# Kernel optimization log

Hardware: AMD Instinct MI355X
Metric: run time of the kernel (lower is better)

## Reference

```python
import math
import jax, jax.numpy as jnp
import numpy as np

BH, S, DK = 64, 1024, 64   # batch*heads, seq_len, head dim
FG, FL = 32, 32            # global / local enrichment feature dims
H, B = 16, 4               # mask layout [heads, batch, seq]


def setup_inputs() -> dict:
    key = jax.random.key(0)
    k1, k2, k3, k4, k5, k6 = jax.random.split(key, 6)
    return {
        "query": jax.random.normal(k1, (BH, S, DK), dtype=jnp.float32),
        "key": jax.random.normal(k2, (BH, S, DK), dtype=jnp.float32),
        "value": jax.random.normal(k3, (BH, S, DK), dtype=jnp.float32),
        "local_f": jax.random.normal(k4, (BH, S, FL), dtype=jnp.float32),
        "global_f": jax.random.normal(k5, (BH, S, FG), dtype=jnp.float32),
        "mask": jax.random.randint(k6, (H, B, S), 0, 2, dtype=jnp.int32),
    }


def reference(query, key, value, local_f, global_f, mask):
    dk = query.shape[-1]
    # enrich q/k with global then local features (matches torch concat order)
    pq = jnp.concatenate([query, global_f, local_f], axis=2)   # [BH, S, dk+fg+fl]
    pk = jnp.concatenate([key, global_f, local_f], axis=2)
    scores = jnp.einsum("bqd,bkd->bqk", pq, pk) / math.sqrt(dk)  # [BH, S, S]
    # mask [H, B, S] -> [H*B, S] -> broadcast over query positions
    m = mask.reshape(-1, mask.shape[-1])[:, None, :]            # [H*B, 1, S]
    scores = jnp.where(m == 1, jnp.float32(-1e9), scores)
    attn = jax.nn.softmax(scores, axis=-1)
    return jnp.einsum("bqk,bkd->bqd", attn, value)              # [BH, S, dk]
```

## Files before the change

kernel.cpp:

```cpp
#include <hip/hip_runtime.h>
#include <hip/hip_bf16.h>


#define BHn 64
#define Sn  1024
#define NT  16
#define KSTR 144
#define VSTR 72
#define KTILE (64*KSTR*2)
#define VTILE (64*VSTR*2)
#define OSTR 68
#define SMEMB (128*OSTR*4 + 512)

typedef __attribute__((ext_vector_type(8)))  __bf16 bf16x8;
typedef __attribute__((ext_vector_type(16))) float  f32x16;
typedef __attribute__((ext_vector_type(4)))  unsigned int u32x4;

__device__ __forceinline__ unsigned f2bf1(float a){
    union { float f; unsigned u; } c; c.f = a;
    return (c.u + 0x7fffu + ((c.u >> 16) & 1u)) >> 16;
}
__device__ __forceinline__ unsigned f2bf2(float a, float b){
    return f2bf1(a) | (f2bf1(b) << 16);
}
__device__ __forceinline__ unsigned pkbf(float a, float b){
    return __builtin_amdgcn_perm(__builtin_bit_cast(unsigned, b),
                                 __builtin_bit_cast(unsigned, a), 0x07060302u);
}
__device__ __forceinline__ void gld_lds16(const void* g, void* l){
    __builtin_amdgcn_global_load_lds(
        (const __attribute__((address_space(1))) unsigned int*)g,
        (__attribute__((address_space(3))) unsigned int*)l, 16, 0, 0);
}

__global__ __launch_bounds__(256)
void attn_prep(const float* __restrict__ K, const float* __restrict__ V,
               const float* __restrict__ LF, const float* __restrict__ GF,
               const int* __restrict__ M,
               unsigned short* __restrict__ Kp, unsigned short* __restrict__ Vp)
{
    const int tid = threadIdx.x;
    const int bh = blockIdx.x >> 4, ti = blockIdx.x & 15, kb = ti*64;
    unsigned short* ktg = Kp + (size_t)(bh*NT + ti) * (64*KSTR);
    unsigned int*   vtg = (unsigned int*)(Vp + (size_t)(bh*NT + ti) * (64*VSTR));

    #pragma unroll
    for (int i=0;i<2;i++){
        int idx = tid + 256*i, row = idx>>3, c = idx&7;
        const float* s = K + ((size_t)bh*Sn + kb + row)*64 + c*8;
        float4 f0 = *(const float4*)s, f1 = *(const float4*)(s+4);
        u32x4 w; w[0]=f2bf2(f0.x,f0.y); w[1]=f2bf2(f0.z,f0.w);
        w[2]=f2bf2(f1.x,f1.y); w[3]=f2bf2(f1.z,f1.w);
        *(u32x4*)(ktg + row*KSTR + c*8) = w;
    }
    {
        int row = tid>>2, c = tid&3;
        const float* s = GF + ((size_t)bh*Sn + kb + row)*32 + c*8;
        float4 f0 = *(const float4*)s, f1 = *(const float4*)(s+4);
        u32x4 w; w[0]=f2bf2(f0.x,f0.y); w[1]=f2bf2(f0.z,f0.w);
        w[2]=f2bf2(f1.x,f1.y); w[3]=f2bf2(f1.z,f1.w);
        *(u32x4*)(ktg + row*KSTR + 64 + c*8) = w;
    }
    {
        int row = tid>>2, c = tid&3;
        const float* s = LF + ((size_t)bh*Sn + kb + row)*32 + c*8;
        float4 f0 = *(const float4*)s, f1 = *(const float4*)(s+4);
        u32x4 w; w[0]=f2bf2(f0.x,f0.y); w[1]=f2bf2(f0.z,f0.w);
        w[2]=f2bf2(f1.x,f1.y); w[3]=f2bf2(f1.z,f1.w);
        *(u32x4*)(ktg + row*KSTR + 96 + c*8) = w;
    }
    if (tid < 64){
        int mv = M[(size_t)bh*Sn + kb + tid];
        u32x4 w; w[0] = (mv == 1) ? 0x0000ceacu : 0u;
        w[1]=0u; w[2]=0u; w[3]=0u;
        *(u32x4*)(ktg + tid*KSTR + 128) = w;
        u32x4 z; z[0]=0u; z[1]=0u; z[2]=0u; z[3]=0u;
        *(u32x4*)(ktg + tid*KSTR + 136) = z;
    }
    {
        int d = tid & 63, g = tid >> 6;
        const float* vb = V + ((size_t)bh*Sn + kb + 16*g)*64 + d;
        const int pm[16] = {0,1,2,3, 8,9,10,11, 4,5,6,7, 12,13,14,15};
        unsigned w[8];
        #pragma unroll
        for (int m=0;m<8;m++)
            w[m] = f2bf2(vb[(size_t)pm[2*m]*64], vb[(size_t)pm[2*m+1]*64]);
        u32x4 a, b;
        a[0]=w[0]; a[1]=w[1]; a[2]=w[2]; a[3]=w[3];
        b[0]=w[4]; b[1]=w[5]; b[2]=w[6]; b[3]=w[7];
        *(u32x4*)(vtg + d*36 + g*8)     = a;
        *(u32x4*)(vtg + d*36 + g*8 + 4) = b;
    }
}

__global__ __launch_bounds__(512, 4)
void attn_main(const float* __restrict__ Q, const unsigned short* __restrict__ Kp,
               const unsigned short* __restrict__ Vp,
               const float* __restrict__ GF, const float* __restrict__ LF,
               float* __restrict__ O)
{
    __shared__ __align__(16) unsigned char smem[SMEMB];
    unsigned short* kt_s = (unsigned short*)smem;
    unsigned short* vt_s = (unsigned short*)(smem + KTILE);

    const int tid  = threadIdx.x;
    const int wave = tid >> 6, lane = tid & 63;
    const int l31  = lane & 31, h = lane >> 5;
    const int qh   = wave >> 1;
    const int kp   = wave & 1;
    const int bh = blockIdx.x & 63;
    const int qb = blockIdx.x >> 6;
    const float SCL = 0.18033688011112042f;

    const int qrow = qb*128 + qh*32 + l31;
    u32x4 qf[9];
    #pragma unroll
    for (int dc = 0; dc < 8; dc++){
        const int cb = dc*16 + 8*h;
        const float* src;
        if (cb < 64)      src = Q  + ((size_t)bh*Sn + qrow)*64 + cb;
        else if (cb < 96) src = GF + ((size_t)bh*Sn + qrow)*32 + (cb - 64);
        else              src = LF + ((size_t)bh*Sn + qrow)*32 + (cb - 96);
        float4 f0 = *(const float4*)src;
        float4 f1 = *(const float4*)(src + 4);
        qf[dc][0] = f2bf2(f0.x*SCL, f0.y*SCL);
        qf[dc][1] = f2bf2(f0.z*SCL, f0.w*SCL);
        qf[dc][2] = f2bf2(f1.x*SCL, f1.y*SCL);
        qf[dc][3] = f2bf2(f1.z*SCL, f1.w*SCL);
    }
    qf[8][0] = h ? 0u : 0x00003f80u;
    qf[8][1] = 0u; qf[8][2] = 0u; qf[8][3] = 0u;

    f32x16 oacc[2];
    #pragma unroll
    for (int dt=0; dt<2; dt++)
        #pragma unroll
        for (int r=0; r<16; r++) oacc[dt][r] = 0.f;
    float lrun = 0.f;

    for (int t = 0; t < NT; t++){
        __syncthreads();
        const unsigned char* gK = (const unsigned char*)Kp + (size_t)(bh*NT + t)*KTILE;
        const unsigned char* gV = (const unsigned char*)Vp + (size_t)(bh*NT + t)*VTILE;
        #pragma unroll
        for (int i=0;i<4;i++){
            int c = wave + 8*i;
            if (c < 18)      gld_lds16(gK + (size_t)c*1024 + lane*16, smem + c*1024);
            else if (c < 27) gld_lds16(gV + (size_t)(c-18)*1024 + lane*16,
                                       smem + KTILE + (size_t)(c-18)*1024);
        }
        __syncthreads();

        f32x16 acc;
        #pragma unroll
        for (int r=0;r<16;r++) acc[r] = 0.f;
        #pragma unroll
        for (int dc=0; dc<9; dc++){
            u32x4 ar = *(const u32x4*)(kt_s + (kp*32 + l31)*KSTR + dc*16 + 8*h);
            acc = __builtin_amdgcn_mfma_f32_32x32x16_bf16(
                    __builtin_bit_cast(bf16x8, ar),
                    __builtin_bit_cast(bf16x8, qf[dc]), acc, 0, 0, 0);
        }

        float rs = 0.f;
        #pragma unroll
        for (int r=0;r<16;r++){
            float p = __builtin_amdgcn_exp2f(acc[r]);
            acc[r] = p; rs += p;
        }
        lrun += rs;

        unsigned pk[8];
        #pragma unroll
        for (int i=0;i<8;i++) pk[i] = pkbf(acc[2*i], acc[2*i+1]);
        u32x4 b0, b1;
        b0[0]=pk[0]; b0[1]=pk[1]; b0[2]=pk[2]; b0[3]=pk[3];
        b1[0]=pk[4]; b1[1]=pk[5]; b1[2]=pk[6]; b1[3]=pk[7];

        #pragma unroll
        for (int dt=0;dt<2;dt++){
            u32x4 va0 = *(const u32x4*)(vt_s + (dt*32 + l31)*VSTR + kp*32 + 8*h);
            u32x4 va1 = *(const u32x4*)(vt_s + (dt*32 + l31)*VSTR + kp*32 + 16 + 8*h);
            oacc[dt] = __builtin_amdgcn_mfma_f32_32x32x16_bf16(
                    __builtin_bit_cast(bf16x8, va0),
                    __builtin_bit_cast(bf16x8, b0), oacc[dt], 0, 0, 0);
            oacc[dt] = __builtin_amdgcn_mfma_f32_32x32x16_bf16(
                    __builtin_bit_cast(bf16x8, va1),
                    __builtin_bit_cast(bf16x8, b1), oacc[dt], 0, 0, 0);
        }
    }

    __syncthreads();
    float lw = lrun + __shfl_xor(lrun, 32, 64);
    float* s1 = (float*)smem;
    float* s2 = (float*)(smem + 128*OSTR*4);
    if (kp == 1){
        #pragma unroll
        for (int dt=0;dt<2;dt++)
            #pragma unroll
            for (int rg=0;rg<4;rg++){
                float4 w;
                w.x = oacc[dt][rg*4+0]; w.y = oacc[dt][rg*4+1];
                w.z = oacc[dt][rg*4+2]; w.w = oacc[dt][rg*4+3];
                *(float4*)(s1 + (qh*32 + l31)*OSTR + dt*32 + rg*8 + 4*h) = w;
            }
        if (h == 0) s2[qh*32 + l31] = lw;
    }
    __syncthreads();
    if (kp == 0){
        float inv = 1.0f / (lw + s2[qh*32 + l31]);
        #pragma unroll
        for (int dt=0;dt<2;dt++)
            #pragma unroll
            for (int rg=0;rg<4;rg++){
                float* p = s1 + (qh*32 + l31)*OSTR + dt*32 + rg*8 + 4*h;
                float4 w = *(float4*)p;
                w.x = (w.x + oacc[dt][rg*4+0])*inv;
                w.y = (w.y + oacc[dt][rg*4+1])*inv;
                w.z = (w.z + oacc[dt][rg*4+2])*inv;
                w.w = (w.w + oacc[dt][rg*4+3])*inv;
                *(float4*)p = w;
            }
    }
    __syncthreads();
    #pragma unroll
    for (int i=0;i<4;i++){
        int idx = tid + 512*i, r = idx>>4, c = idx&15;
        *(float4*)(O + ((size_t)bh*Sn + qb*128 + r)*64 + c*4) =
            *(const float4*)(s1 + r*OSTR + c*4);
    }
}

extern "C" void kernel_launch(void* const* d_in, const int* in_sizes, int n_in,
                              void* d_out, int out_size, void* d_ws, size_t ws_size,
                              hipStream_t stream) {
    const float* Q  = (const float*)d_in[0];
    const float* K  = (const float*)d_in[1];
    const float* V  = (const float*)d_in[2];
    const float* LF = (const float*)d_in[3];
    const float* GF = (const float*)d_in[4];
    const int*   M  = (const int*)d_in[5];
    float* O = (float*)d_out;

    unsigned short* Kp = (unsigned short*)d_ws;
    unsigned short* Vp = Kp + (size_t)BHn*NT*64*KSTR;

    attn_prep<<<dim3(BHn*NT), dim3(256), 0, stream>>>(K, V, LF, GF, M, Kp, Vp);
    attn_main<<<dim3(BHn*(Sn/128)), dim3(512), 0, stream>>>(Q, Kp, Vp, GF, LF, O);
}
```

Measured before the change: 148.7 us.

## Double-buffer K/V tile loads into LDS and widen K row stride

Splits shared memory into two K/V buffers. The global-to-LDS load for tile t+1 is issued before computing on tile t, with a vmcnt wait at the end of each iteration, so load latency overlaps with the MFMA work. Also pads the packed K row stride from 144 to 152 elements, likely to reduce LDS bank conflicts, and zero-fills the extra padding in the prep kernel. LDS use per block grows to about 57 KB, which limits how many blocks fit on a CU.

```diff
diff --git a/kernel.cpp b/kernel.cpp
--- a/kernel.cpp
+++ b/kernel.cpp
@@ -5,12 +5,13 @@
 #define BHn 64
 #define Sn  1024
 #define NT  16
-#define KSTR 144
+#define KSTR 152
 #define VSTR 72
 #define KTILE (64*KSTR*2)
 #define VTILE (64*VSTR*2)
+#define BUFSZ (KTILE+VTILE)
 #define OSTR 68
-#define SMEMB (128*OSTR*4 + 512)
+#define WAIT_VM0 0x0F70
 
 typedef __attribute__((ext_vector_type(8)))  __bf16 bf16x8;
 typedef __attribute__((ext_vector_type(16))) float  f32x16;
@@ -76,6 +77,7 @@
         *(u32x4*)(ktg + tid*KSTR + 128) = w;
         u32x4 z; z[0]=0u; z[1]=0u; z[2]=0u; z[3]=0u;
         *(u32x4*)(ktg + tid*KSTR + 136) = z;
+        *(u32x4*)(ktg + tid*KSTR + 144) = z;
     }
     {
         int d = tid & 63, g = tid >> 6;
@@ -99,10 +101,7 @@
                const float* __restrict__ GF, const float* __restrict__ LF,
                float* __restrict__ O)
 {
-    __shared__ __align__(16) unsigned char smem[SMEMB];
-    unsigned short* kt_s = (unsigned short*)smem;
-    unsigned short* vt_s = (unsigned short*)(smem + KTILE);
-
+    __shared__ __align__(16) unsigned char smem[2*BUFSZ];
     const int tid  = threadIdx.x;
     const int wave = tid >> 6, lane = tid & 63;
     const int l31  = lane & 31, h = lane >> 5;
@@ -138,18 +137,37 @@
         for (int r=0; r<16; r++) oacc[dt][r] = 0.f;
     float lrun = 0.f;
 
-    for (int t = 0; t < NT; t++){
-        __syncthreads();
-        const unsigned char* gK = (const unsigned char*)Kp + (size_t)(bh*NT + t)*KTILE;
-        const unsigned char* gV = (const unsigned char*)Vp + (size_t)(bh*NT + t)*VTILE;
+    const unsigned char* gKb = (const unsigned char*)Kp + (size_t)bh*NT*KTILE;
+    const unsigned char* gVb = (const unsigned char*)Vp + (size_t)bh*NT*VTILE;
+
+    {
         #pragma unroll
         for (int i=0;i<4;i++){
             int c = wave + 8*i;
-            if (c < 18)      gld_lds16(gK + (size_t)c*1024 + lane*16, smem + c*1024);
-            else if (c < 27) gld_lds16(gV + (size_t)(c-18)*1024 + lane*16,
-                                       smem + KTILE + (size_t)(c-18)*1024);
-        }
+            if (c < 19)      gld_lds16(gKb + (size_t)c*1024 + lane*16, smem + c*1024);
+            else if (c < 28) gld_lds16(gVb + (size_t)(c-19)*1024 + lane*16,
+                                       smem + KTILE + (size_t)(c-19)*1024);
+        }
+    }
+    __builtin_amdgcn_s_waitcnt(WAIT_VM0);
+
+    for (int t = 0; t < NT; t++){
+        unsigned char* cur = smem + (size_t)(t&1)*BUFSZ;
+        unsigned char* nxt = smem + (size_t)((t+1)&1)*BUFSZ;
         __syncthreads();
+        if (t+1 < NT){
+            const unsigned char* gK = gKb + (size_t)(t+1)*KTILE;
+            const unsigned char* gV = gVb + (size_t)(t+1)*VTILE;
+            #pragma unroll
+            for (int i=0;i<4;i++){
+                int c = wave + 8*i;
+                if (c < 19)      gld_lds16(gK + (size_t)c*1024 + lane*16, nxt + c*1024);
+                else if (c < 28) gld_lds16(gV + (size_t)(c-19)*1024 + lane*16,
+                                           nxt + KTILE + (size_t)(c-19)*1024);
+            }
+        }
+        unsigned short* kt_s = (unsigned short*)cur;
+        unsigned short* vt_s = (unsigned short*)(cur + KTILE);
 
         f32x16 acc;
         #pragma unroll
@@ -188,6 +206,8 @@
                     __builtin_bit_cast(bf16x8, va1),
                     __builtin_bit_cast(bf16x8, b1), oacc[dt], 0, 0, 0);
         }
+
+        __builtin_amdgcn_s_waitcnt(WAIT_VM0);
     }
 
     __syncthreads();
```

Result: faster. 143.5 us (-3.5%).

## Pre-swizzle K/V into MFMA fragment images and load directly to registers

Applied to the files above, without the earlier changes.

The prep kernel now writes K and V as per-lane MFMA fragment images, so the main kernel reads each operand with one coalesced 16-byte global load straight into registers. This removes the per-tile LDS staging and both block-wide barriers per tile. The main kernel also shrinks to 256 threads covering 64 query rows, which doubles the grid. In exchange, each block re-reads K/V from global/L2 with no LDS sharing between the two query-half waves, so L2 traffic per query row rises.

```diff
diff --git a/kernel.cpp b/kernel.cpp
--- a/kernel.cpp
+++ b/kernel.cpp
@@ -5,12 +5,7 @@
 #define BHn 64
 #define Sn  1024
 #define NT  16
-#define KSTR 144
-#define VSTR 72
-#define KTILE (64*KSTR*2)
-#define VTILE (64*VSTR*2)
 #define OSTR 68
-#define SMEMB (128*OSTR*4 + 512)
 
 typedef __attribute__((ext_vector_type(8)))  __bf16 bf16x8;
 typedef __attribute__((ext_vector_type(16))) float  f32x16;
@@ -26,83 +21,71 @@
 __device__ __forceinline__ unsigned pkbf(float a, float b){
     return __builtin_amdgcn_perm(__builtin_bit_cast(unsigned, b),
                                  __builtin_bit_cast(unsigned, a), 0x07060302u);
-}
-__device__ __forceinline__ void gld_lds16(const void* g, void* l){
-    __builtin_amdgcn_global_load_lds(
-        (const __attribute__((address_space(1))) unsigned int*)g,
-        (__attribute__((address_space(3))) unsigned int*)l, 16, 0, 0);
 }
 
 __global__ __launch_bounds__(256)
 void attn_prep(const float* __restrict__ K, const float* __restrict__ V,
                const float* __restrict__ LF, const float* __restrict__ GF,
                const int* __restrict__ M,
-               unsigned short* __restrict__ Kp, unsigned short* __restrict__ Vp)
+               unsigned int* __restrict__ Kimg, unsigned int* __restrict__ Vimg)
 {
     const int tid = threadIdx.x;
-    const int bh = blockIdx.x >> 4, ti = blockIdx.x & 15, kb = ti*64;
-    unsigned short* ktg = Kp + (size_t)(bh*NT + ti) * (64*KSTR);
-    unsigned int*   vtg = (unsigned int*)(Vp + (size_t)(bh*NT + ti) * (64*VSTR));
-
-    #pragma unroll
-    for (int i=0;i<2;i++){
-        int idx = tid + 256*i, row = idx>>3, c = idx&7;
-        const float* s = K + ((size_t)bh*Sn + kb + row)*64 + c*8;
-        float4 f0 = *(const float4*)s, f1 = *(const float4*)(s+4);
-        u32x4 w; w[0]=f2bf2(f0.x,f0.y); w[1]=f2bf2(f0.z,f0.w);
-        w[2]=f2bf2(f1.x,f1.y); w[3]=f2bf2(f1.z,f1.w);
-        *(u32x4*)(ktg + row*KSTR + c*8) = w;
-    }
-    {
-        int row = tid>>2, c = tid&3;
-        const float* s = GF + ((size_t)bh*Sn + kb + row)*32 + c*8;
-        float4 f0 = *(const float4*)s, f1 = *(const float4*)(s+4);
-        u32x4 w; w[0]=f2bf2(f0.x,f0.y); w[1]=f2bf2(f0.z,f0.w);
-        w[2]=f2bf2(f1.x,f1.y); w[3]=f2bf2(f1.z,f1.w);
-        *(u32x4*)(ktg + row*KSTR + 64 + c*8) = w;
-    }
-    {
-        int row = tid>>2, c = tid&3;
-        const float* s = LF + ((size_t)bh*Sn + kb + row)*32 + c*8;
-        float4 f0 = *(const float4*)s, f1 = *(const float4*)(s+4);
-        u32x4 w; w[0]=f2bf2(f0.x,f0.y); w[1]=f2bf2(f0.z,f0.w);
-        w[2]=f2bf2(f1.x,f1.y); w[3]=f2bf2(f1.z,f1.w);
-        *(u32x4*)(ktg + row*KSTR + 96 + c*8) = w;
-    }
-    if (tid < 64){
-        int mv = M[(size_t)bh*Sn + kb + tid];
-        u32x4 w; w[0] = (mv == 1) ? 0x0000ceacu : 0u;
-        w[1]=0u; w[2]=0u; w[3]=0u;
-        *(u32x4*)(ktg + tid*KSTR + 128) = w;
-        u32x4 z; z[0]=0u; z[1]=0u; z[2]=0u; z[3]=0u;
-        *(u32x4*)(ktg + tid*KSTR + 136) = z;
-    }
-    {
-        int d = tid & 63, g = tid >> 6;
-        const float* vb = V + ((size_t)bh*Sn + kb + 16*g)*64 + d;
-        const int pm[16] = {0,1,2,3, 8,9,10,11, 4,5,6,7, 12,13,14,15};
-        unsigned w[8];
-        #pragma unroll
-        for (int m=0;m<8;m++)
-            w[m] = f2bf2(vb[(size_t)pm[2*m]*64], vb[(size_t)pm[2*m+1]*64]);
-        u32x4 a, b;
-        a[0]=w[0]; a[1]=w[1]; a[2]=w[2]; a[3]=w[3];
-        b[0]=w[4]; b[1]=w[5]; b[2]=w[6]; b[3]=w[7];
-        *(u32x4*)(vtg + d*36 + g*8)     = a;
-        *(u32x4*)(vtg + d*36 + g*8 + 4) = b;
-    }
-}
-
-__global__ __launch_bounds__(512, 4)
-void attn_main(const float* __restrict__ Q, const unsigned short* __restrict__ Kp,
-               const unsigned short* __restrict__ Vp,
+    const int wave = tid >> 6, lane = tid & 63;
+    const int l31 = lane & 31, h = lane >> 5;
+    const int bh = blockIdx.x & 63, t = blockIdx.x >> 6;
+
+    #pragma unroll
+    for (int i = 0; i < 5; i++){
+        int ch = wave + 4*i;
+        if (ch >= 18) break;
+        int kp = ch / 9, dc = ch % 9;
+        int r  = t*64 + kp*32 + l31;
+        unsigned int* out = Kimg +
+            ((size_t)((bh*NT + t)*2 + kp)*9 + dc)*256 + lane*4;
+        u32x4 w;
+        if (dc < 8){
+            int c0 = dc*16 + 8*h;
+            const float* s;
+            if (c0 < 64)      s = K  + ((size_t)bh*Sn + r)*64 + c0;
+            else if (c0 < 96) s = GF + ((size_t)bh*Sn + r)*32 + (c0 - 64);
+            else              s = LF + ((size_t)bh*Sn + r)*32 + (c0 - 96);
+            float4 f0 = *(const float4*)s, f1 = *(const float4*)(s + 4);
+            w[0] = f2bf2(f0.x, f0.y); w[1] = f2bf2(f0.z, f0.w);
+            w[2] = f2bf2(f1.x, f1.y); w[3] = f2bf2(f1.z, f1.w);
+        } else {
+            w[1] = 0u; w[2] = 0u; w[3] = 0u;
+            w[0] = (h == 0 && M[(size_t)bh*Sn + r] == 1) ? 0x0000ceacu : 0u;
+        }
+        *(u32x4*)out = w;
+    }
+
+    #pragma unroll
+    for (int i = 0; i < 2; i++){
+        int ch = wave + 4*i;
+        int kp = ch >> 2, dt = (ch >> 1) & 1, j = ch & 1;
+        int d  = dt*32 + l31;
+        int rb = t*64 + kp*32 + j*16;
+        const int off0 = h ? 4 : 0, off1 = h ? 12 : 8;
+        const float* vb = V + ((size_t)bh*Sn + rb)*64 + d;
+        u32x4 w;
+        w[0] = f2bf2(vb[(size_t)(off0+0)*64], vb[(size_t)(off0+1)*64]);
+        w[1] = f2bf2(vb[(size_t)(off0+2)*64], vb[(size_t)(off0+3)*64]);
+        w[2] = f2bf2(vb[(size_t)(off1+0)*64], vb[(size_t)(off1+1)*64]);
+        w[3] = f2bf2(vb[(size_t)(off1+2)*64], vb[(size_t)(off1+3)*64]);
+        unsigned int* out = Vimg +
+            ((size_t)((bh*NT + t)*2 + kp)*4 + dt*2 + j)*256 + lane*4;
+        *(u32x4*)out = w;
+    }
+}
+
+__global__ __launch_bounds__(256, 3)
+void attn_main(const float* __restrict__ Q, const unsigned int* __restrict__ Kimg,
+               const unsigned int* __restrict__ Vimg,
                const float* __restrict__ GF, const float* __restrict__ LF,
                float* __restrict__ O)
 {
-    __shared__ __align__(16) unsigned char smem[SMEMB];
-    unsigned short* kt_s = (unsigned short*)smem;
-    unsigned short* vt_s = (unsigned short*)(smem + KTILE);
-
+    __shared__ float s1[64*OSTR];
+    __shared__ float s2[64];
     const int tid  = threadIdx.x;
     const int wave = tid >> 6, lane = tid & 63;
     const int l31  = lane & 31, h = lane >> 5;
@@ -112,7 +95,7 @@
     const int qb = blockIdx.x >> 6;
     const float SCL = 0.18033688011112042f;
 
-    const int qrow = qb*128 + qh*32 + l31;
+    const int qrow = qb*64 + qh*32 + l31;
     u32x4 qf[9];
     #pragma unroll
     for (int dc = 0; dc < 8; dc++){
@@ -138,27 +121,25 @@
         for (int r=0; r<16; r++) oacc[dt][r] = 0.f;
     float lrun = 0.f;
 
+    const unsigned int* kc = Kimg + (size_t)((bh*NT)*2 + kp)*9*256 + lane*4;
+    const unsigned int* vc = Vimg + (size_t)((bh*NT)*2 + kp)*4*256 + lane*4;
+
     for (int t = 0; t < NT; t++){
-        __syncthreads();
-        const unsigned char* gK = (const unsigned char*)Kp + (size_t)(bh*NT + t)*KTILE;
-        const unsigned char* gV = (const unsigned char*)Vp + (size_t)(bh*NT + t)*VTILE;
-        #pragma unroll
-        for (int i=0;i<4;i++){
-            int c = wave + 8*i;
-            if (c < 18)      gld_lds16(gK + (size_t)c*1024 + lane*16, smem + c*1024);
-            else if (c < 27) gld_lds16(gV + (size_t)(c-18)*1024 + lane*16,
-                                       smem + KTILE + (size_t)(c-18)*1024);
-        }
-        __syncthreads();
+        const unsigned int* kt = kc + (size_t)t*2*9*256;
+        const unsigned int* vt = vc + (size_t)t*2*4*256;
+
+        u32x4 va[4];
+        #pragma unroll
+        for (int c=0;c<4;c++) va[c] = *(const u32x4*)(vt + c*256);
 
         f32x16 acc;
         #pragma unroll
         for (int r=0;r<16;r++) acc[r] = 0.f;
         #pragma unroll
         for (int dc=0; dc<9; dc++){
-            u32x4 ar = *(const u32x4*)(kt_s + (kp*32 + l31)*KSTR + dc*16 + 8*h);
+            u32x4 kf = *(const u32x4*)(kt + dc*256);
             acc = __builtin_amdgcn_mfma_f32_32x32x16_bf16(
-                    __builtin_bit_cast(bf16x8, ar),
+                    __builtin_bit_cast(bf16x8, kf),
                     __builtin_bit_cast(bf16x8, qf[dc]), acc, 0, 0, 0);
         }
 
@@ -170,30 +151,25 @@
         }
         lrun += rs;
 
-        unsigned pk[8];
-        #pragma unroll
-        for (int i=0;i<8;i++) pk[i] = pkbf(acc[2*i], acc[2*i+1]);
         u32x4 b0, b1;
-        b0[0]=pk[0]; b0[1]=pk[1]; b0[2]=pk[2]; b0[3]=pk[3];
-        b1[0]=pk[4]; b1[1]=pk[5]; b1[2]=pk[6]; b1[3]=pk[7];
+        #pragma unroll
+        for (int i=0;i<4;i++){
+            b0[i] = pkbf(acc[2*i],   acc[2*i+1]);
+            b1[i] = pkbf(acc[2*i+8], acc[2*i+9]);
+        }
 
         #pragma unroll
         for (int dt=0;dt<2;dt++){
-            u32x4 va0 = *(const u32x4*)(vt_s + (dt*32 + l31)*VSTR + kp*32 + 8*h);
-            u32x4 va1 = *(const u32x4*)(vt_s + (dt*32 + l31)*VSTR + kp*32 + 16 + 8*h);
             oacc[dt] = __builtin_amdgcn_mfma_f32_32x32x16_bf16(
-                    __builtin_bit_cast(bf16x8, va0),
+                    __builtin_bit_cast(bf16x8, va[dt*2]),
                     __builtin_bit_cast(bf16x8, b0), oacc[dt], 0, 0, 0);
             oacc[dt] = __builtin_amdgcn_mfma_f32_32x32x16_bf16(
-                    __builtin_bit_cast(bf16x8, va1),
+                    __builtin_bit_cast(bf16x8, va[dt*2+1]),
                     __builtin_bit_cast(bf16x8, b1), oacc[dt], 0, 0, 0);
         }
     }
 
-    __syncthreads();
     float lw = lrun + __shfl_xor(lrun, 32, 64);
-    float* s1 = (float*)smem;
-    float* s2 = (float*)(smem + 128*OSTR*4);
     if (kp == 1){
         #pragma unroll
         for (int dt=0;dt<2;dt++)
@@ -225,8 +201,8 @@
     __syncthreads();
     #pragma unroll
     for (int i=0;i<4;i++){
-        int idx = tid + 512*i, r = idx>>4, c = idx&15;
-        *(float4*)(O + ((size_t)bh*Sn + qb*128 + r)*64 + c*4) =
+        int idx = tid + 256*i, r = idx>>4, c = idx&15;
+        *(float4*)(O + ((size_t)bh*Sn + qb*64 + r)*64 + c*4) =
             *(const float4*)(s1 + r*OSTR + c*4);
     }
 }
@@ -242,9 +218,9 @@
     const int*   M  = (const int*)d_in[5];
     float* O = (float*)d_out;
 
-    unsigned short* Kp = (unsigned short*)d_ws;
-    unsigned short* Vp = Kp + (size_t)BHn*NT*64*KSTR;
-
-    attn_prep<<<dim3(BHn*NT), dim3(256), 0, stream>>>(K, V, LF, GF, M, Kp, Vp);
-    attn_main<<<dim3(BHn*(Sn/128)), dim3(512), 0, stream>>>(Q, Kp, Vp, GF, LF, O);
-}
+    unsigned int* Kimg = (unsigned int*)d_ws;
+    unsigned int* Vimg = Kimg + (size_t)BHn*NT*2*9*256;
+
+    attn_prep<<<dim3(BHn*NT), dim3(256), 0, stream>>>(K, V, LF, GF, M, Kimg, Vimg);
+    attn_main<<<dim3(BHn*(Sn/64)), dim3(256), 0, stream>>>(Q, Kimg, Vimg, GF, LF, O);
+}
```

New measurement: 157.4 us. +5.9%, slower.
